# Kernel tuning notes

Hardware: AMD Instinct MI355X
Metric: run time of the kernel (lower is better)

## Reference

```python
import jax, jax.numpy as jnp
import numpy as np

DIM, NH, T_MAX = 1024, 16, 2048
HD = DIM // NH
EPS = 1e-6


def _rope_tables(T, hd, dtype=jnp.float32):
    inv_freq = 1.0 / (10000.0 ** (jnp.arange(0, hd, 2, dtype=jnp.float32) / hd))
    t = jnp.arange(T, dtype=jnp.float32)
    freqs = jnp.outer(t, inv_freq)                 # [T, hd/2]
    emb = jnp.concatenate([freqs, freqs], axis=-1)  # [T, hd]
    return jnp.cos(emb).astype(dtype), jnp.sin(emb).astype(dtype)


def _rotate_half(x):
    x1, x2 = jnp.split(x, 2, axis=-1)
    return jnp.concatenate([-x2, x1], axis=-1)


def _rmsnorm(x, g):
    rms = jnp.sqrt(jnp.mean(x * x, axis=-1, keepdims=True) + EPS)
    return x / rms * g


def setup_inputs() -> dict:
    key = jax.random.key(0)
    ks = jax.random.split(key, 10)
    B, T, C = 4, 2048, DIM
    s = 1.0 / np.sqrt(C)
    x = jax.random.normal(ks[0], (B, T, C), dtype=jnp.float32)
    mask = jnp.tril(jnp.ones((T, T), dtype=jnp.int32))[None, None, :, :]
    wq = jax.random.normal(ks[1], (C, C), jnp.float32) * s
    wk = jax.random.normal(ks[2], (C, C), jnp.float32) * s
    wv = jax.random.normal(ks[3], (C, C), jnp.float32) * s
    wo = jax.random.normal(ks[4], (C, C), jnp.float32) * s
    w1 = jax.random.normal(ks[5], (C, 4 * C), jnp.float32) * s
    w2 = jax.random.normal(ks[6], (4 * C, C), jnp.float32) * (1.0 / np.sqrt(4 * C))
    w3 = jax.random.normal(ks[7], (C, 4 * C), jnp.float32) * s
    g1 = jnp.ones((C,), jnp.float32)
    g2 = jnp.ones((C,), jnp.float32)
    return {"x": x, "mask": mask, "g1": g1, "wq": wq, "wk": wk, "wv": wv,
            "wo": wo, "g2": g2, "w1": w1, "w2": w2, "w3": w3}


def reference(x, mask, g1, wq, wk, wv, wo, g2, w1, w2, w3):
    B, T, C = x.shape
    scale = HD ** -0.5
    # --- attention sublayer ---
    h = _rmsnorm(x, g1)
    q = (h @ wq).reshape(B, T, NH, HD)
    k = (h @ wk).reshape(B, T, NH, HD)
    v = (h @ wv).reshape(B, T, NH, HD)
    cos, sin = _rope_tables(T, HD, x.dtype)
    cos = cos[None, :, None, :]
    sin = sin[None, :, None, :]
    q = q * cos + _rotate_half(q) * sin
    k = k * cos + _rotate_half(k) * sin
    attn = jnp.einsum("bthd,bshd->bhts", q, k) * scale  # [B,H,T,T]
    attn = jnp.where(mask == 0, -jnp.inf, attn)
    attn = jax.nn.softmax(attn, axis=-1)
    o = jnp.einsum("bhts,bshd->bthd", attn, v).reshape(B, T, C)
    x = x + o @ wo
    # --- SwiGLU FFN sublayer ---
    h = _rmsnorm(x, g2)
    x = x + (jax.nn.silu(h @ w1) * (h @ w3)) @ w2
    return x
```

## Files before the change

### kernel.cpp

```cpp
#include <hip/hip_runtime.h>
#include <cstdint>

typedef unsigned short u16;
typedef __attribute__((ext_vector_type(8))) short bf16x8;
typedef __attribute__((ext_vector_type(4))) float f32x4;

__device__ __forceinline__ u16 f2b(float f) {
  union { float f; unsigned u; } c; c.f = f;
  unsigned u = c.u;
  return (u16)((u + 0x7FFFu + ((u >> 16) & 1u)) >> 16);
}
__device__ __forceinline__ float b2f(u16 b) {
  union { unsigned u; float f; } c; c.u = ((unsigned)b) << 16;
  return c.f;
}

typedef __attribute__((address_space(1))) void gv_t;
typedef __attribute__((address_space(3))) void lv_t;
__device__ __forceinline__ void gload_lds16(const void* g, void* l) {
  __builtin_amdgcn_global_load_lds((gv_t*)g, (lv_t*)l, 16, 0, 0);
}

__global__ void transpose_f2b(const float* __restrict__ in, u16* __restrict__ out,
                              int R, int C) {
  __shared__ float t[32][33];
  const int c0 = blockIdx.x * 32, r0 = blockIdx.y * 32;
  const int tx = threadIdx.x, ty = threadIdx.y;
#pragma unroll
  for (int i = 0; i < 4; ++i)
    t[ty + 8 * i][tx] = in[(size_t)(r0 + ty + 8 * i) * C + c0 + tx];
  __syncthreads();
#pragma unroll
  for (int i = 0; i < 4; ++i)
    out[(size_t)(c0 + ty + 8 * i) * R + r0 + tx] = f2b(t[tx][ty + 8 * i]);
}

__global__ __launch_bounds__(256) void rmsnorm_k(const float* __restrict__ x,
                                                 const float* __restrict__ g,
                                                 u16* __restrict__ out) {
  const int row = blockIdx.x, tid = threadIdx.x;
  const float4 v = ((const float4*)x)[(size_t)row * 256 + tid];
  float ss = v.x * v.x + v.y * v.y + v.z * v.z + v.w * v.w;
#pragma unroll
  for (int off = 1; off < 64; off <<= 1) ss += __shfl_xor(ss, off, 64);
  __shared__ float red[4];
  if ((tid & 63) == 0) red[tid >> 6] = ss;
  __syncthreads();
  const float mean = (red[0] + red[1] + red[2] + red[3]) * (1.0f / 1024.0f);
  const float rinv = 1.0f / sqrtf(mean + 1e-6f);
  const float4 gv = ((const float4*)g)[tid];
  u16* o = out + (size_t)row * 1024 + tid * 4;
  o[0] = f2b(v.x * rinv * gv.x);
  o[1] = f2b(v.y * rinv * gv.y);
  o[2] = f2b(v.z * rinv * gv.z);
  o[3] = f2b(v.w * rinv * gv.w);
}

__global__ __launch_bounds__(256) void rope_k(u16* __restrict__ qkv) {
  const int i = blockIdx.x * 256 + threadIdx.x;
  const int d = i & 31;
  const int h = (i >> 5) & 15;
  const int bt = i >> 9;
  const int t = bt & 2047;
  const float inv = exp2f((float)d * -0.4152410118609203f);
  const float th = (float)t * inv;
  float s, c;
  sincosf(th, &s, &c);
  size_t base = (size_t)bt * 3072 + h * 64 + d;
#pragma unroll
  for (int half = 0; half < 2; ++half) {
    const float x1 = b2f(qkv[base]);
    const float x2 = b2f(qkv[base + 32]);
    qkv[base]      = f2b(x1 * c - x2 * s);
    qkv[base + 32] = f2b(x2 * c + x1 * s);
    base += 1024;
  }
}

__global__ void vtrans_k(const u16* __restrict__ qkv, u16* __restrict__ VT) {
  __shared__ u16 tl[32][34];
  const int t0 = blockIdx.x * 32;
  const int bh = blockIdx.y >> 1;
  const int d0 = (blockIdx.y & 1) * 32;
  const int b = bh >> 4, h = bh & 15;
  const int tx = threadIdx.x, ty = threadIdx.y;
  const u16* src = qkv + (size_t)(b * 2048 + t0) * 3072 + 2048 + h * 64 + d0;
#pragma unroll
  for (int i = 0; i < 4; ++i)
    tl[ty + 8 * i][tx] = src[(size_t)(ty + 8 * i) * 3072 + tx];
  __syncthreads();
  u16* dst = VT + ((size_t)bh * 64 + d0) * 2048 + t0;
#pragma unroll
  for (int i = 0; i < 4; ++i)
    dst[(size_t)(ty + 8 * i) * 2048 + tx] = tl[tx][ty + 8 * i];
}

template <int EPI>
__global__ __launch_bounds__(256)
void gemm_bt(const u16* __restrict__ A, const u16* __restrict__ BT,
             void* __restrict__ Cout, const float* __restrict__ resid,
             int M, int N, int K, int lda) {
  __shared__ alignas(16) u16 As[128 * 32];
  __shared__ alignas(16) u16 Bs[128 * 32];
  const int tid = threadIdx.x;
  const int wave = tid >> 6, lane = tid & 63;
  const int wr = wave >> 1, wc = wave & 1;
  const int l15 = lane & 15, quad = lane >> 4;
  const int bm = blockIdx.x * 128, bn = blockIdx.y * 128;

  f32x4 acc[4][4];
#pragma unroll
  for (int i = 0; i < 4; ++i)
#pragma unroll
    for (int j = 0; j < 4; ++j) acc[i][j] = (f32x4){0.f, 0.f, 0.f, 0.f};

  const int srow = wave * 32 + (lane >> 2);
  const int scol = (lane & 3) * 8;
  const u16* gA0 = A + (size_t)(bm + srow) * lda + scol;
  const u16* gA1 = gA0 + (size_t)16 * lda;
  const u16* gB0 = BT + (size_t)(bn + srow) * K + scol;
  const u16* gB1 = gB0 + (size_t)16 * K;
  u16* lA0 = As + wave * 1024; u16* lA1 = lA0 + 512;
  u16* lB0 = Bs + wave * 1024; u16* lB1 = lB0 + 512;

  const u16* pa = As + (wr * 64 + l15) * 32 + quad * 8;
  const u16* pb = Bs + (wc * 64 + l15) * 32 + quad * 8;

  for (int kt = 0; kt < K; kt += 32) {
    gload_lds16(gA0 + kt, lA0);
    gload_lds16(gA1 + kt, lA1);
    gload_lds16(gB0 + kt, lB0);
    gload_lds16(gB1 + kt, lB1);
    __syncthreads();
    bf16x8 af[4], bfv[4];
#pragma unroll
    for (int i = 0; i < 4; ++i) af[i] = *(const bf16x8*)(pa + i * 512);
#pragma unroll
    for (int j = 0; j < 4; ++j) bfv[j] = *(const bf16x8*)(pb + j * 512);
#pragma unroll
    for (int i = 0; i < 4; ++i)
#pragma unroll
      for (int j = 0; j < 4; ++j)
        acc[i][j] = __builtin_amdgcn_mfma_f32_16x16x32_bf16(af[i], bfv[j], acc[i][j], 0, 0, 0);
    __syncthreads();
  }

#pragma unroll
  for (int i = 0; i < 4; ++i) {
    const int gr = bm + wr * 64 + i * 16 + quad * 4;
#pragma unroll
    for (int j = 0; j < 4; ++j) {
      const int gc = bn + wc * 64 + j * 16 + l15;
#pragma unroll
      for (int r = 0; r < 4; ++r) {
        const size_t off = (size_t)(gr + r) * N + gc;
        if (EPI == 0) {
          ((u16*)Cout)[off] = f2b(acc[i][j][r]);
        } else {
          ((float*)Cout)[off] = resid[off] + acc[i][j][r];
        }
      }
    }
  }
}

template <int EPI>
__global__ __launch_bounds__(512, 2)
void gemm256(const u16* __restrict__ A, const u16* __restrict__ BT,
             void* __restrict__ Cout, const float* __restrict__ resid,
             int M, int N, int K, int lda) {
  __shared__ alignas(16) u16 LDS[65536];
  char* const ldsc = (char*)LDS;
  const int tid = threadIdx.x;
  const int wave = tid >> 6, lane = tid & 63;
  const int wr = wave >> 2, wc = wave & 3;
  const int l15 = lane & 15, quad = lane >> 4;
  const int bm = blockIdx.x * 256, bn = blockIdx.y * 256;
  const int NT = K >> 6;
  const int NIT = NT >> 1;

  const int swz = (l15 & 8) << 2;
  const int aoff = (((wr * 64 + l15) * 64 + quad * 16) ^ swz);
  const int boff = (((wc * 32 + l15) * 64 + quad * 16) ^ swz) + 65536;

  const int kperm = ((lane & 3) ^ ((lane >> 5) << 1)) * 8;
  const u16* sA = A + (size_t)(bm + wave * 16 + (lane >> 2)) * lda + kperm;
  const u16* sB = BT + (size_t)(bn + wave * 16 + (lane >> 2)) * K + kperm;
  const size_t hA = (size_t)128 * lda;
  const size_t hB = (size_t)128 * K;
  const int dstW = wave * 1024;

  f32x4 acc[8][4];
#pragma unroll
  for (int m = 0; m < 8; ++m)
#pragma unroll
    for (int n = 0; n < 4; ++n) acc[m][n] = (f32x4){0.f, 0.f, 0.f, 0.f};
  bf16x8 a[4][2], b[2][2];

#define STAGE(kt_, slot_, buf_)                                               \
  if ((kt_) < NT) {                                                           \
    const u16* s_ = (((slot_) & 1) ? sB + ((size_t)((slot_) >> 1)) * hB       \
                                   : sA + ((size_t)((slot_) >> 1)) * hA) +    \
                    (size_t)(kt_) * 64;                                       \
    char* d_ = ldsc + (((slot_) & 1) ? 65536 : 0) + (buf_) * 32768 +          \
               ((slot_) >> 1) * 16384 + dstW;                                 \
    gload_lds16(s_, d_);                                                      \
    gload_lds16(s_ + 32, d_ + 8192);                                          \
  }

#define LOAD_A(mh_, buf_)                                                     \
  _Pragma("unroll") for (int mf = 0; mf < 4; ++mf)                            \
      _Pragma("unroll") for (int kk = 0; kk < 2; ++kk)                        \
          a[mf][kk] = *(const bf16x8*)(ldsc + aoff + (buf_) * 32768 +         \
                                       (mh_) * 16384 + kk * 8192 + mf * 1024);

#define LOAD_B(nh_, buf_)                                                     \
  _Pragma("unroll") for (int nf = 0; nf < 2; ++nf)                            \
      _Pragma("unroll") for (int kk = 0; kk < 2; ++kk)                        \
          b[nf][kk] = *(const bf16x8*)(ldsc + boff + (buf_) * 32768 +         \
                                       (nh_) * 16384 + kk * 8192 + nf * 1024);

#define MMA(mh_, nh_)                                                         \
  __builtin_amdgcn_s_setprio(1);                                              \
  _Pragma("unroll") for (int mf = 0; mf < 4; ++mf)                            \
      _Pragma("unroll") for (int nf = 0; nf < 2; ++nf)                        \
          _Pragma("unroll") for (int kk = 0; kk < 2; ++kk)                    \
              acc[(mh_) * 4 + mf][(nh_) * 2 + nf] =                           \
                  __builtin_amdgcn_mfma_f32_16x16x32_bf16(                    \
                      a[mf][kk], b[nf][kk],                                   \
                      acc[(mh_) * 4 + mf][(nh_) * 2 + nf], 0, 0, 0);          \
  __builtin_amdgcn_s_setprio(0);

#define BAR() __builtin_amdgcn_s_barrier()
#define DRAIN_LGKM()                                                          \
  {                                                                           \
    asm volatile("s_waitcnt lgkmcnt(0)" ::: "memory");                        \
    __builtin_amdgcn_sched_barrier(0);                                        \
  }

  STAGE(0, 0, 0); STAGE(0, 1, 0); STAGE(0, 2, 0); STAGE(0, 3, 0);
  STAGE(1, 0, 1); STAGE(1, 1, 1);
  asm volatile("s_waitcnt vmcnt(4)" ::: "memory");
  BAR();

  for (int i = 0; i < NIT; ++i) {
    const int t = 2 * i;
    LOAD_A(0, 0); LOAD_B(0, 0); STAGE(t + 1, 2, 1);
    BAR(); DRAIN_LGKM(); MMA(0, 0); BAR();
    LOAD_B(1, 0); STAGE(t + 1, 3, 1);
    BAR(); DRAIN_LGKM(); MMA(0, 1); BAR();
    LOAD_A(1, 0); LOAD_B(0, 0); STAGE(t + 2, 0, 0);
    BAR(); DRAIN_LGKM(); MMA(1, 0); BAR();
    LOAD_B(1, 0); STAGE(t + 2, 1, 0);
    BAR(); DRAIN_LGKM(); MMA(1, 1);
    if (i == NIT - 1) { asm volatile("s_waitcnt vmcnt(0)" ::: "memory"); }
    else              { asm volatile("s_waitcnt vmcnt(4)" ::: "memory"); }
    BAR();
    LOAD_A(0, 1); LOAD_B(0, 1); STAGE(t + 2, 2, 0);
    BAR(); DRAIN_LGKM(); MMA(0, 0); BAR();
    LOAD_B(1, 1); STAGE(t + 2, 3, 0);
    BAR(); DRAIN_LGKM(); MMA(0, 1); BAR();
    LOAD_A(1, 1); LOAD_B(0, 1); STAGE(t + 3, 0, 1);
    BAR(); DRAIN_LGKM(); MMA(1, 0); BAR();
    LOAD_B(1, 1); STAGE(t + 3, 1, 1);
    BAR(); DRAIN_LGKM(); MMA(1, 1);
    if (i < NIT - 1) { asm volatile("s_waitcnt vmcnt(4)" ::: "memory"); }
    BAR();
  }
#undef STAGE
#undef LOAD_A
#undef LOAD_B
#undef MMA

#pragma unroll
  for (int m = 0; m < 8; ++m) {
    const int gr = bm + (m >> 2) * 128 + wr * 64 + (m & 3) * 16 + quad * 4;
#pragma unroll
    for (int n = 0; n < 4; ++n) {
      const int gc = bn + (n >> 1) * 128 + wc * 32 + (n & 1) * 16 + l15;
#pragma unroll
      for (int r = 0; r < 4; ++r) {
        const size_t off = (size_t)(gr + r) * N + gc;
        if (EPI == 0) {
          ((u16*)Cout)[off] = f2b(acc[m][n][r]);
        } else {
          ((float*)Cout)[off] = resid[off] + acc[m][n][r];
        }
      }
    }
  }
#undef BAR
#undef DRAIN_LGKM
}

template <int EPI>
__global__ __launch_bounds__(512, 2)
void gemm256n(const u16* __restrict__ A, const u16* __restrict__ BT,
              void* __restrict__ Cout, const float* __restrict__ resid,
              int M, int N, int K, int lda) {
  __shared__ alignas(16) u16 LDS[49152];
  char* const ldsc = (char*)LDS;
  const int tid = threadIdx.x;
  const int wave = tid >> 6, lane = tid & 63;
  const int wr = wave >> 2, wc = wave & 3;
  const int l15 = lane & 15, quad = lane >> 4;
  const int bm = blockIdx.x * 256, bn = blockIdx.y * 128;
  const int NT = K >> 6;

  const int swz = (l15 & 8) << 2;
  const int aoff = (((wr * 64 + l15) * 64 + quad * 16) ^ swz);
  const int boff = (((wc * 32 + l15) * 64 + quad * 16) ^ swz) + 65536;

  const int kperm = ((lane & 3) ^ ((lane >> 5) << 1)) * 8;
  const u16* sA = A + (size_t)(bm + wave * 16 + (lane >> 2)) * lda + kperm;
  const u16* sB = BT + (size_t)(bn + wave * 16 + (lane >> 2)) * K + kperm;
  const size_t hA = (size_t)128 * lda;
  const int dstW = wave * 1024;

  f32x4 acc[8][2];
#pragma unroll
  for (int m = 0; m < 8; ++m)
#pragma unroll
    for (int n = 0; n < 2; ++n) acc[m][n] = (f32x4){0.f, 0.f, 0.f, 0.f};
  bf16x8 a[4][2], b[2][2];

#define STAGE_A(kt_, half_, buf_)                                             \
  if ((kt_) < NT) {                                                           \
    const u16* s_ = sA + (size_t)(half_) * hA + (size_t)(kt_) * 64;           \
    char* d_ = ldsc + (buf_) * 32768 + (half_) * 16384 + dstW;                \
    gload_lds16(s_, d_);                                                      \
    gload_lds16(s_ + 32, d_ + 8192);                                          \
  }
#define STAGE_B(kt_, buf_)                                                    \
  if ((kt_) < NT) {                                                           \
    const u16* s_ = sB + (size_t)(kt_) * 64;                                  \
    char* d_ = ldsc + 65536 + (buf_) * 16384 + dstW;                          \
    gload_lds16(s_, d_);                                                      \
    gload_lds16(s_ + 32, d_ + 8192);                                          \
  }
#define LOAD_A(mh_, buf_)                                                     \
  _Pragma("unroll") for (int mf = 0; mf < 4; ++mf)                            \
      _Pragma("unroll") for (int kk = 0; kk < 2; ++kk)                        \
          a[mf][kk] = *(const bf16x8*)(ldsc + aoff + (buf_) * 32768 +         \
                                       (mh_) * 16384 + kk * 8192 + mf * 1024);
#define LOAD_B(buf_)                                                          \
  _Pragma("unroll") for (int nf = 0; nf < 2; ++nf)                            \
      _Pragma("unroll") for (int kk = 0; kk < 2; ++kk)                        \
          b[nf][kk] = *(const bf16x8*)(ldsc + boff + (buf_) * 16384 +         \
                                       kk * 8192 + nf * 1024);
#define MMA(mh_)                                                              \
  __builtin_amdgcn_s_setprio(1);                                              \
  _Pragma("unroll") for (int mf = 0; mf < 4; ++mf)                            \
      _Pragma("unroll") for (int nf = 0; nf < 2; ++nf)                        \
          _Pragma("unroll") for (int kk = 0; kk < 2; ++kk)                    \
              acc[(mh_) * 4 + mf][nf] =                                       \
                  __builtin_amdgcn_mfma_f32_16x16x32_bf16(                    \
                      a[mf][kk], b[nf][kk], acc[(mh_) * 4 + mf][nf], 0, 0, 0);\
  __builtin_amdgcn_s_setprio(0);
#define BAR() __builtin_amdgcn_s_barrier()
#define DRAIN_LGKM()                                                          \
  {                                                                           \
    asm volatile("s_waitcnt lgkmcnt(0)" ::: "memory");                        \
    __builtin_amdgcn_sched_barrier(0);                                        \
  }

  STAGE_A(0, 0, 0); STAGE_B(0, 0);
  STAGE_A(0, 1, 0);
  STAGE_A(1, 0, 1); STAGE_B(1, 1);
  asm volatile("s_waitcnt vmcnt(6)" ::: "memory");
  BAR();

  for (int t = 0; t < NT; ++t) {
    const int bsel = t & 1;
    LOAD_A(0, bsel); LOAD_B(bsel);
    STAGE_A(t + 1, 1, bsel ^ 1);
    BAR(); DRAIN_LGKM(); MMA(0);
    if (t == NT - 1) { asm volatile("s_waitcnt vmcnt(0)" ::: "memory"); }
    else             { asm volatile("s_waitcnt vmcnt(6)" ::: "memory"); }
    BAR();
    LOAD_A(1, bsel);
    STAGE_A(t + 2, 0, bsel); STAGE_B(t + 2, bsel);
    BAR(); DRAIN_LGKM(); MMA(1);
    if (t == NT - 2)     { asm volatile("s_waitcnt vmcnt(2)" ::: "memory"); }
    else if (t < NT - 2) { asm volatile("s_waitcnt vmcnt(6)" ::: "memory"); }
    BAR();
  }
#undef STAGE_A
#undef STAGE_B
#undef LOAD_A
#undef LOAD_B
#undef MMA
#undef BAR
#undef DRAIN_LGKM

#pragma unroll
  for (int m = 0; m < 8; ++m) {
    const int gr = bm + (m >> 2) * 128 + wr * 64 + (m & 3) * 16 + quad * 4;
#pragma unroll
    for (int n = 0; n < 2; ++n) {
      const int gc = bn + wc * 32 + n * 16 + l15;
#pragma unroll
      for (int r = 0; r < 4; ++r) {
        const size_t off = (size_t)(gr + r) * N + gc;
        if (EPI == 0) {
          ((u16*)Cout)[off] = f2b(acc[m][n][r]);
        } else {
          ((float*)Cout)[off] = resid[off] + acc[m][n][r];
        }
      }
    }
  }
}

__global__ __launch_bounds__(256)
void attn_kernel(const u16* __restrict__ QKV, const u16* __restrict__ VT,
                 u16* __restrict__ O, float* __restrict__ Opart,
                 float* __restrict__ Spart) {
  const int T = 2048, stQ = 3072;
  const int tid = threadIdx.x, wave = tid >> 6, lane = tid & 63;
  const int l15 = lane & 15, quad = lane >> 4;

  const int xi = (int)blockIdx.x;
  const bool split = (xi < 22);
  const int qt = split ? (15 - (xi >> 1)) : (26 - xi);
  const int chunk = split ? (xi & 1) : 0;
  const int len = split ? (qt + 1) : (2 * qt + 2);
  const int kt0 = chunk * (qt + 1);
  const int ktEnd = kt0 + len;

  const int qb0 = qt * 128;
  const int bh = blockIdx.y, b = bh >> 4, h = bh & 15;
  const float sc2 = 0.125f * 1.44269504088896f;
  const float M0 = 32.0f;

  __shared__ alignas(16) u16 Kf[2][8 * 512];
  __shared__ alignas(16) u16 Vf[2][8 * 512];
  __shared__ alignas(16) u16 Pl[4][2][16 * 72];

  const u16* Qb  = QKV + (size_t)b * T * stQ + h * 64;
  const u16* Kb  = Qb + 1024;
  const u16* VTb = VT + (size_t)bh * 64 * T;

  const int r0 = qb0 + wave * 16;
  const int r1 = r0 + 64;
  const u16* qp0 = Qb + (size_t)(r0 + l15) * stQ + quad * 8;
  const u16* qp1 = Qb + (size_t)(r1 + l15) * stQ + quad * 8;
  const bf16x8 qf00 = *(const bf16x8*)qp0;
  const bf16x8 qf01 = *(const bf16x8*)(qp0 + 32);
  const bf16x8 qf10 = *(const bf16x8*)qp1;
  const bf16x8 qf11 = *(const bf16x8*)(qp1 + 32);

  bf16x8 ones;
#pragma unroll
  for (int j = 0; j < 8; ++j) ones[j] = (short)0x3F80;

  const u16* kS = Kb + (size_t)(wave * 16 + l15) * stQ + quad * 8;
  const u16* vS = VTb + (size_t)(wave * 16 + l15) * T + quad * 8;

  f32x4 o0[4], o1[4], sum0, sum1;
#pragma unroll
  for (int c = 0; c < 4; ++c) {
    o0[c] = (f32x4){0.f, 0.f, 0.f, 0.f};
    o1[c] = (f32x4){0.f, 0.f, 0.f, 0.f};
  }
  sum0 = (f32x4){0.f, 0.f, 0.f, 0.f};
  sum1 = (f32x4){0.f, 0.f, 0.f, 0.f};

  u16* pw0 = &Pl[wave][0][0];
  u16* pw1 = &Pl[wave][1][0];

  gload_lds16(kS + (size_t)(kt0 * 64) * stQ,      &Kf[0][(wave * 2 + 0) * 512]);
  gload_lds16(kS + (size_t)(kt0 * 64) * stQ + 32, &Kf[0][(wave * 2 + 1) * 512]);
  gload_lds16(vS + (size_t)(kt0 * 64),            &Vf[0][(wave * 2 + 0) * 512]);
  gload_lds16(vS + (size_t)(kt0 * 64) + 32,       &Vf[0][(wave * 2 + 1) * 512]);

  for (int kt = kt0; kt < ktEnd; ++kt) {
    const int kb0 = kt * 64;
    const int buf = (kt - kt0) & 1;
    __builtin_amdgcn_sched_barrier(0);
    if (kt + 1 < ktEnd) {
      const size_t kb1 = (size_t)(kb0 + 64);
      gload_lds16(kS + kb1 * stQ,      &Kf[buf ^ 1][(wave * 2 + 0) * 512]);
      gload_lds16(kS + kb1 * stQ + 32, &Kf[buf ^ 1][(wave * 2 + 1) * 512]);
      gload_lds16(vS + kb1,            &Vf[buf ^ 1][(wave * 2 + 0) * 512]);
      gload_lds16(vS + kb1 + 32,       &Vf[buf ^ 1][(wave * 2 + 1) * 512]);
      asm volatile("s_waitcnt vmcnt(4)" ::: "memory");
    } else {
      asm volatile("s_waitcnt vmcnt(0)" ::: "memory");
    }
    __builtin_amdgcn_s_barrier();
    __builtin_amdgcn_sched_barrier(0);

    bf16x8 kf[8], vf[8];
#pragma unroll
    for (int g = 0; g < 8; ++g) {
      kf[g] = *(const bf16x8*)(&Kf[buf][g * 512 + lane * 8]);
      vf[g] = *(const bf16x8*)(&Vf[buf][g * 512 + lane * 8]);
    }

    const bool act0 = (kb0 <= r0 + 15);

    {
      f32x4 s[4];
      __builtin_amdgcn_s_setprio(1);
#pragma unroll
      for (int jj = 0; jj < 4; ++jj) {
        s[jj] = (f32x4){0.f, 0.f, 0.f, 0.f};
        s[jj] = __builtin_amdgcn_mfma_f32_16x16x32_bf16(qf10, kf[jj * 2 + 0], s[jj], 0, 0, 0);
        s[jj] = __builtin_amdgcn_mfma_f32_16x16x32_bf16(qf11, kf[jj * 2 + 1], s[jj], 0, 0, 0);
      }
      __builtin_amdgcn_s_setprio(0);
      if (kb0 + 63 > r1) {
#pragma unroll
        for (int jj = 0; jj < 4; ++jj)
#pragma unroll
          for (int r = 0; r < 4; ++r) {
            const bool msk = (kb0 + jj * 16 + l15) > (r1 + quad * 4 + r);
            const float a = msk ? -1e30f : (s[jj][r] * sc2 - M0);
            pw1[(quad * 4 + r) * 72 + jj * 16 + l15] = f2b(exp2f(a));
          }
      } else {
#pragma unroll
        for (int jj = 0; jj < 4; ++jj)
#pragma unroll
          for (int r = 0; r < 4; ++r)
            pw1[(quad * 4 + r) * 72 + jj * 16 + l15] =
                f2b(exp2f(s[jj][r] * sc2 - M0));
      }
    }
    if (act0) {
      f32x4 s[4];
      __builtin_amdgcn_s_setprio(1);
#pragma unroll
      for (int jj = 0; jj < 4; ++jj) {
        s[jj] = (f32x4){0.f, 0.f, 0.f, 0.f};
        s[jj] = __builtin_amdgcn_mfma_f32_16x16x32_bf16(qf00, kf[jj * 2 + 0], s[jj], 0, 0, 0);
        s[jj] = __builtin_amdgcn_mfma_f32_16x16x32_bf16(qf01, kf[jj * 2 + 1], s[jj], 0, 0, 0);
      }
      __builtin_amdgcn_s_setprio(0);
      if (kb0 + 63 > r0) {
#pragma unroll
        for (int jj = 0; jj < 4; ++jj)
#pragma unroll
          for (int r = 0; r < 4; ++r) {
            const bool msk = (kb0 + jj * 16 + l15) > (r0 + quad * 4 + r);
            const float a = msk ? -1e30f : (s[jj][r] * sc2 - M0);
            pw0[(quad * 4 + r) * 72 + jj * 16 + l15] = f2b(exp2f(a));
          }
      } else {
#pragma unroll
        for (int jj = 0; jj < 4; ++jj)
#pragma unroll
          for (int r = 0; r < 4; ++r)
            pw0[(quad * 4 + r) * 72 + jj * 16 + l15] =
                f2b(exp2f(s[jj][r] * sc2 - M0));
      }
    }

    const bf16x8 pf10 = *(const bf16x8*)(pw1 + l15 * 72 + quad * 8);
    const bf16x8 pf11 = *(const bf16x8*)(pw1 + l15 * 72 + 32 + quad * 8);
    __builtin_amdgcn_s_setprio(1);
#pragma unroll
    for (int c = 0; c < 4; ++c) {
      o1[c] = __builtin_amdgcn_mfma_f32_16x16x32_bf16(pf10, vf[c * 2 + 0], o1[c], 0, 0, 0);
      o1[c] = __builtin_amdgcn_mfma_f32_16x16x32_bf16(pf11, vf[c * 2 + 1], o1[c], 0, 0, 0);
    }
    sum1 = __builtin_amdgcn_mfma_f32_16x16x32_bf16(pf10, ones, sum1, 0, 0, 0);
    sum1 = __builtin_amdgcn_mfma_f32_16x16x32_bf16(pf11, ones, sum1, 0, 0, 0);
    __builtin_amdgcn_s_setprio(0);
    if (act0) {
      const bf16x8 pf00 = *(const bf16x8*)(pw0 + l15 * 72 + quad * 8);
      const bf16x8 pf01 = *(const bf16x8*)(pw0 + l15 * 72 + 32 + quad * 8);
      __builtin_amdgcn_s_setprio(1);
#pragma unroll
      for (int c = 0; c < 4; ++c) {
        o0[c] = __builtin_amdgcn_mfma_f32_16x16x32_bf16(pf00, vf[c * 2 + 0], o0[c], 0, 0, 0);
        o0[c] = __builtin_amdgcn_mfma_f32_16x16x32_bf16(pf01, vf[c * 2 + 1], o0[c], 0, 0, 0);
      }
      sum0 = __builtin_amdgcn_mfma_f32_16x16x32_bf16(pf00, ones, sum0, 0, 0, 0);
      sum0 = __builtin_amdgcn_mfma_f32_16x16x32_bf16(pf01, ones, sum0, 0, 0, 0);
      __builtin_amdgcn_s_setprio(0);
    }
    __builtin_amdgcn_s_barrier();
  }

  if (split) {
    const int pi = (bh * 11 + (qt - 5)) * 2 + chunk;
    float* Po = Opart + (size_t)pi * 8192;
    float* Ps = Spart + (size_t)pi * 128;
    const int lr0 = wave * 16 + quad * 4;
#pragma unroll
    for (int c = 0; c < 4; ++c)
#pragma unroll
      for (int r = 0; r < 4; ++r) {
        Po[(lr0 + r) * 64 + c * 16 + l15]      = o0[c][r];
        Po[(64 + lr0 + r) * 64 + c * 16 + l15] = o1[c][r];
      }
    if (l15 == 0) {
#pragma unroll
      for (int r = 0; r < 4; ++r) {
        Ps[lr0 + r]      = sum0[r];
        Ps[64 + lr0 + r] = sum1[r];
      }
    }
  } else {
    float i0[4], i1[4];
#pragma unroll
    for (int r = 0; r < 4; ++r) { i0[r] = 1.f / sum0[r]; i1[r] = 1.f / sum1[r]; }
    u16* op0 = O + ((size_t)(b * T) + r0 + quad * 4) * 1024 + h * 64 + l15;
    u16* op1 = O + ((size_t)(b * T) + r1 + quad * 4) * 1024 + h * 64 + l15;
#pragma unroll
    for (int c = 0; c < 4; ++c)
#pragma unroll
      for (int r = 0; r < 4; ++r) {
        op0[(size_t)r * 1024 + c * 16] = f2b(o0[c][r] * i0[r]);
        op1[(size_t)r * 1024 + c * 16] = f2b(o1[c][r] * i1[r]);
      }
  }
}

__global__ __launch_bounds__(256)
void attn_combine(const float* __restrict__ Opart, const float* __restrict__ Spart,
                  u16* __restrict__ O) {
  const int sp = blockIdx.x;
  const int bh = sp / 11, qt = 5 + (sp % 11);
  const int b = bh >> 4, h = bh & 15;
  const int t = threadIdx.x;
  const int row = t >> 1, ch = (t & 1) * 32;
  const size_t p0 = (size_t)(2 * sp) * 8192, p1 = p0 + 8192;
  const float s = Spart[(size_t)(2 * sp) * 128 + row] +
                  Spart[(size_t)(2 * sp) * 128 + 128 + row];
  const float inv = 1.f / s;
  const float4* A  = (const float4*)(Opart + p0 + row * 64 + ch);
  const float4* Bv = (const float4*)(Opart + p1 + row * 64 + ch);
  u16* op = O + ((size_t)(b * 2048) + qt * 128 + row) * 1024 + h * 64 + ch;
#pragma unroll
  for (int j = 0; j < 8; ++j) {
    const float4 a = A[j], bb = Bv[j];
    op[j * 4 + 0] = f2b((a.x + bb.x) * inv);
    op[j * 4 + 1] = f2b((a.y + bb.y) * inv);
    op[j * 4 + 2] = f2b((a.z + bb.z) * inv);
    op[j * 4 + 3] = f2b((a.w + bb.w) * inv);
  }
}

__global__ __launch_bounds__(256) void gate_k(u16* __restrict__ a13) {
  const size_t i = (size_t)blockIdx.x * 256 + threadIdx.x;
  const size_t row = i >> 9, c8 = (i & 511) * 8;
  u16* p1v = a13 + row * 8192 + c8;
  const u16* p3v = p1v + 4096;
  uint4 u1 = *(uint4*)p1v;
  const uint4 u3 = *(const uint4*)p3v;
  u16* p1 = (u16*)&u1;
  const u16* p3 = (const u16*)&u3;
#pragma unroll
  for (int j = 0; j < 8; ++j) {
    const float a = b2f(p1[j]);
    const float g = b2f(p3[j]);
    const float s = a / (1.f + __expf(-a));
    p1[j] = f2b(s * g);
  }
  *(uint4*)p1v = u1;
}

extern "C" void kernel_launch(void* const* d_in, const int* in_sizes, int n_in,
                              void* d_out, int out_size, void* d_ws, size_t ws_size,
                              hipStream_t stream) {
  const float* x  = (const float*)d_in[0];
  const float* g1 = (const float*)d_in[2];
  const float* wq = (const float*)d_in[3];
  const float* wk = (const float*)d_in[4];
  const float* wv = (const float*)d_in[5];
  const float* wo = (const float*)d_in[6];
  const float* g2 = (const float*)d_in[7];
  const float* w1 = (const float*)d_in[8];
  const float* w2 = (const float*)d_in[9];
  const float* w3 = (const float*)d_in[10];
  float* out = (float*)d_out;

  const int T = 2048, NH = 16, B = 4;
  const int M = B * T;
  const size_t MB = 1ull << 20;

  char* ws = (char*)d_ws;
  u16* hb    = (u16*)(ws);
  u16* wqkvT = (u16*)(ws + 16 * MB);
  u16* woT   = (u16*)(ws + 22 * MB);
  u16* w13T  = (u16*)(ws + 24 * MB);
  u16* w2T   = (u16*)(ws + 40 * MB);
  u16* qkv   = (u16*)(ws + 48 * MB);
  u16* VT    = (u16*)(ws + 96 * MB);
  u16* Ob    = (u16*)(ws + 112 * MB);
  u16* a13   = (u16*)(ws + 48 * MB);
  float* Opart = (float*)(ws + 128 * MB);
  float* Spart = Opart + (size_t)1408 * 8192;

  const dim3 tb(32, 8);
  transpose_f2b<<<dim3(32, 32),  tb, 0, stream>>>(wq, wqkvT,              1024, 1024);
  transpose_f2b<<<dim3(32, 32),  tb, 0, stream>>>(wk, wqkvT + 1024*1024,  1024, 1024);
  transpose_f2b<<<dim3(32, 32),  tb, 0, stream>>>(wv, wqkvT + 2048*1024,  1024, 1024);
  transpose_f2b<<<dim3(32, 32),  tb, 0, stream>>>(wo, woT, 1024, 1024);
  transpose_f2b<<<dim3(128, 32), tb, 0, stream>>>(w1, w13T,               1024, 4096);
  transpose_f2b<<<dim3(128, 32), tb, 0, stream>>>(w3, w13T + 4096*1024,   1024, 4096);
  transpose_f2b<<<dim3(32, 128), tb, 0, stream>>>(w2, w2T, 4096, 1024);

  rmsnorm_k<<<M, 256, 0, stream>>>(x, g1, hb);

  gemm256<0><<<dim3(32, 12), 512, 0, stream>>>(hb, wqkvT, qkv, nullptr, M, 3072, 1024, 1024);

  rope_k<<<16384, 256, 0, stream>>>(qkv);
  vtrans_k<<<dim3(64, 128), tb, 0, stream>>>(qkv, VT);

  attn_kernel<<<dim3(27, B * NH), 256, 0, stream>>>(qkv, VT, Ob, Opart, Spart);
  attn_combine<<<dim3(704), 256, 0, stream>>>(Opart, Spart, Ob);

  gemm256n<1><<<dim3(32, 8), 512, 0, stream>>>(Ob, woT, out, x, M, 1024, 1024, 1024);

  rmsnorm_k<<<M, 256, 0, stream>>>(out, g2, hb);

  gemm256<0><<<dim3(32, 32), 512, 0, stream>>>(hb, w13T, a13, nullptr, M, 8192, 1024, 1024);

  gate_k<<<16384, 256, 0, stream>>>(a13);

  gemm256n<1><<<dim3(32, 8), 512, 0, stream>>>(a13, w2T, out, out, M, 1024, 4096, 8192);
}
```

Before: 672.9 us.

## Restructure gemm256 main loop into two MMA phases per k-tile with full B preload

The 256x256 GEMM main loop now loads all four B fragments per k-tile at once and issues two larger MMA phases per tile (one per A half) instead of four smaller phases. This halves the number of barriers and LDS drains per k-tile and reorders the global-to-LDS staging to match, with adjusted vmcnt waits. It doubles the B fragment registers, which may pressure occupancy under the 512x2 launch bounds. The changed wait counts and staging order carry a risk of LDS races.

```diff
diff --git a/kernel.cpp b/kernel.cpp
--- a/kernel.cpp
+++ b/kernel.cpp
@@ -177,7 +177,6 @@
   const int l15 = lane & 15, quad = lane >> 4;
   const int bm = blockIdx.x * 256, bn = blockIdx.y * 256;
   const int NT = K >> 6;
-  const int NIT = NT >> 1;
 
   const int swz = (l15 & 8) << 2;
   const int aoff = (((wr * 64 + l15) * 64 + quad * 16) ^ swz);
@@ -195,7 +194,7 @@
   for (int m = 0; m < 8; ++m)
 #pragma unroll
     for (int n = 0; n < 4; ++n) acc[m][n] = (f32x4){0.f, 0.f, 0.f, 0.f};
-  bf16x8 a[4][2], b[2][2];
+  bf16x8 a[4][2], b[4][2];
 
 #define STAGE(kt_, slot_, buf_)                                               \
   if ((kt_) < NT) {                                                           \
@@ -214,21 +213,22 @@
           a[mf][kk] = *(const bf16x8*)(ldsc + aoff + (buf_) * 32768 +         \
                                        (mh_) * 16384 + kk * 8192 + mf * 1024);
 
-#define LOAD_B(nh_, buf_)                                                     \
-  _Pragma("unroll") for (int nf = 0; nf < 2; ++nf)                            \
-      _Pragma("unroll") for (int kk = 0; kk < 2; ++kk)                        \
-          b[nf][kk] = *(const bf16x8*)(ldsc + boff + (buf_) * 32768 +         \
-                                       (nh_) * 16384 + kk * 8192 + nf * 1024);
-
-#define MMA(mh_, nh_)                                                         \
+#define LOAD_B2(buf_)                                                         \
+  _Pragma("unroll") for (int nh = 0; nh < 2; ++nh)                            \
+      _Pragma("unroll") for (int nf = 0; nf < 2; ++nf)                        \
+          _Pragma("unroll") for (int kk = 0; kk < 2; ++kk)                    \
+              b[nh * 2 + nf][kk] =                                            \
+                  *(const bf16x8*)(ldsc + boff + (buf_) * 32768 +             \
+                                   nh * 16384 + kk * 8192 + nf * 1024);
+
+#define MMA2(mh_)                                                             \
   __builtin_amdgcn_s_setprio(1);                                              \
   _Pragma("unroll") for (int mf = 0; mf < 4; ++mf)                            \
-      _Pragma("unroll") for (int nf = 0; nf < 2; ++nf)                        \
+      _Pragma("unroll") for (int n = 0; n < 4; ++n)                           \
           _Pragma("unroll") for (int kk = 0; kk < 2; ++kk)                    \
-              acc[(mh_) * 4 + mf][(nh_) * 2 + nf] =                           \
+              acc[(mh_) * 4 + mf][n] =                                        \
                   __builtin_amdgcn_mfma_f32_16x16x32_bf16(                    \
-                      a[mf][kk], b[nf][kk],                                   \
-                      acc[(mh_) * 4 + mf][(nh_) * 2 + nf], 0, 0, 0);          \
+                      a[mf][kk], b[n][kk], acc[(mh_) * 4 + mf][n], 0, 0, 0);  \
   __builtin_amdgcn_s_setprio(0);
 
 #define BAR() __builtin_amdgcn_s_barrier()
@@ -238,39 +238,35 @@
     __builtin_amdgcn_sched_barrier(0);                                        \
   }
 
-  STAGE(0, 0, 0); STAGE(0, 1, 0); STAGE(0, 2, 0); STAGE(0, 3, 0);
-  STAGE(1, 0, 1); STAGE(1, 1, 1);
-  asm volatile("s_waitcnt vmcnt(4)" ::: "memory");
+  STAGE(0, 0, 0); STAGE(0, 1, 0); STAGE(0, 3, 0);
+  STAGE(0, 2, 0);
+  STAGE(1, 0, 1); STAGE(1, 1, 1); STAGE(1, 3, 1);
+  asm volatile("s_waitcnt vmcnt(8)" ::: "memory");
   BAR();
 
-  for (int i = 0; i < NIT; ++i) {
-    const int t = 2 * i;
-    LOAD_A(0, 0); LOAD_B(0, 0); STAGE(t + 1, 2, 1);
-    BAR(); DRAIN_LGKM(); MMA(0, 0); BAR();
-    LOAD_B(1, 0); STAGE(t + 1, 3, 1);
-    BAR(); DRAIN_LGKM(); MMA(0, 1); BAR();
-    LOAD_A(1, 0); LOAD_B(0, 0); STAGE(t + 2, 0, 0);
-    BAR(); DRAIN_LGKM(); MMA(1, 0); BAR();
-    LOAD_B(1, 0); STAGE(t + 2, 1, 0);
-    BAR(); DRAIN_LGKM(); MMA(1, 1);
-    if (i == NIT - 1) { asm volatile("s_waitcnt vmcnt(0)" ::: "memory"); }
-    else              { asm volatile("s_waitcnt vmcnt(4)" ::: "memory"); }
+  for (int t = 0; t < NT; ++t) {
+    const int bsel = t & 1;
+    LOAD_A(0, bsel); LOAD_B2(bsel);
+    STAGE(t + 1, 2, bsel ^ 1);
+    BAR(); DRAIN_LGKM(); MMA2(0);
+    if (t == NT - 1) { asm volatile("s_waitcnt vmcnt(0)" ::: "memory"); }
+    else             { asm volatile("s_waitcnt vmcnt(8)" ::: "memory"); }
     BAR();
-    LOAD_A(0, 1); LOAD_B(0, 1); STAGE(t + 2, 2, 0);
-    BAR(); DRAIN_LGKM(); MMA(0, 0); BAR();
-    LOAD_B(1, 1); STAGE(t + 2, 3, 0);
-    BAR(); DRAIN_LGKM(); MMA(0, 1); BAR();
-    LOAD_A(1, 1); LOAD_B(0, 1); STAGE(t + 3, 0, 1);
-    BAR(); DRAIN_LGKM(); MMA(1, 0); BAR();
-    LOAD_B(1, 1); STAGE(t + 3, 1, 1);
-    BAR(); DRAIN_LGKM(); MMA(1, 1);
-    if (i < NIT - 1) { asm volatile("s_waitcnt vmcnt(4)" ::: "memory"); }
-    BAR();
+    LOAD_A(1, bsel);
+    STAGE(t + 2, 0, bsel); STAGE(t + 2, 1, bsel); STAGE(t + 2, 3, bsel);
+    BAR(); DRAIN_LGKM(); MMA2(1);
+    if (t < NT - 2) {
+      asm volatile("s_waitcnt vmcnt(8)" ::: "memory");
+      BAR();
+    } else if (t == NT - 2) {
+      asm volatile("s_waitcnt vmcnt(2)" ::: "memory");
+      BAR();
+    }
   }
 #undef STAGE
 #undef LOAD_A
-#undef LOAD_B
-#undef MMA
+#undef LOAD_B2
+#undef MMA2
 
 #pragma unroll
   for (int m = 0; m < 8; ++m) {
```

After: 674.7 us. Within noise of the previous version (+0.3%).
